# Optimization experiments

Hardware: AMD Instinct MI355X
Metric: run time of the kernel (lower is better)

The kernel has to match this reference:

```python
import jax, jax.numpy as jnp
import numpy as np

B, N, C, O = 512, 64, 256, 256  # batch graphs, agents(nodes), in_ch, out_ch


def _full_graph_edges(n):
    # PyG-style directed upper-triangular edges (j, i+j+1) + self loops,
    # then GCN symmetric normalization with in-degree computed at col.
    src, dst = np.triu_indices(n, k=1)           # src < dst, matches build_edge_index('full')
    loop = np.arange(n)
    row = np.concatenate([src, loop]).astype(np.int32)   # message source
    col = np.concatenate([dst, loop]).astype(np.int32)   # message target (aggregation)
    deg = np.bincount(col, minlength=n).astype(np.float32)
    dis = 1.0 / np.sqrt(deg)
    norm = (dis[row] * dis[col]).astype(np.float32)
    return jnp.asarray(row), jnp.asarray(col), jnp.asarray(norm)


def setup_inputs() -> dict:
    key = jax.random.key(0)
    k1, k2 = jax.random.split(key, 2)
    x = jax.random.normal(k1, (B, N, C), dtype=jnp.float32)
    W = jax.random.normal(k2, (C, O), dtype=jnp.float32) / np.sqrt(C)
    b = jnp.zeros((O,), dtype=jnp.float32)
    return {"x": x, "W": W, "b": b}


def reference(x, W, b):
    # GCNConv: out = D^-1/2 (A + I) D^-1/2 (X W) + b, then ReLU (module forward).
    n = x.shape[1]
    row, col, norm = _full_graph_edges(n)
    xw = jnp.einsum('bnc,co->bno', x, W)                      # [B, N, O]
    msg = xw[:, row, :] * norm[None, :, None]                 # gather along edges [B, E, O]
    agg = jax.vmap(lambda m: jax.ops.segment_sum(m, col, num_segments=n))(msg)  # scatter-add [B, N, O]
    return jax.nn.relu(agg + b)
```

## Files before the change

kernel.cpp:

```cpp
#include <hip/hip_runtime.h>


#define BATCH 512
#define NNODE 64
#define CIN   256
#define COUT  256

typedef __bf16 bf16x8 __attribute__((ext_vector_type(8)));
typedef float  f32x4  __attribute__((ext_vector_type(4)));

#define LGKM_BARRIER() asm volatile("s_waitcnt lgkmcnt(0)\n\ts_barrier" ::: "memory")

__global__ __launch_bounds__(512, 1) void gcn_fused(
    const float* __restrict__ X,
    const float* __restrict__ W,
    const float* __restrict__ bias,
    float* __restrict__ out)
{
    __shared__ uint4 Xs4[2][2048];
    const int tid  = threadIdx.x;
    const int lane = tid & 63;
    const int w    = tid >> 6;
    const int g    = lane >> 4;
    const int c    = lane & 15;
    const int colbase = w * 32;
    const int xg   = blockIdx.x * 2;

    const float* xb0 = X + (size_t)xg * (NNODE * CIN);
    const float* xb1 = xb0 + NNODE * CIN;

    f32x4 pf[8];
#pragma unroll
    for (int i = 0; i < 4; ++i) {
        int ch  = tid + i * 512;
        const f32x4* p = reinterpret_cast<const f32x4*>(
            xb0 + (ch >> 5) * CIN + ((ch & 31) << 3));
        pf[2 * i]     = p[0];
        pf[2 * i + 1] = p[1];
    }

    bf16x8 bfr[8][2];
    {
        const float* Wp = W + colbase + c;
#pragma unroll
        for (int kk = 0; kk < 8; ++kk)
#pragma unroll
            for (int nt = 0; nt < 2; ++nt) {
                bf16x8 t;
#pragma unroll
                for (int j = 0; j < 8; ++j)
                    t[j] = (__bf16)Wp[(size_t)(kk * 32 + g * 8 + j) * COUT + nt * 16];
                bfr[kk][nt] = t;
            }
    }
    float bias_c[2];
#pragma unroll
    for (int nt = 0; nt < 2; ++nt)
        bias_c[nt] = bias[colbase + nt * 16 + c];

#pragma unroll
    for (int i = 0; i < 4; ++i) {
        int ch  = tid + i * 512;
        int row = ch >> 5;
        int c8  = (ch & 31) << 3;
        f32x4 v0 = pf[2 * i], v1 = pf[2 * i + 1];
        bf16x8 h;
        h[0] = (__bf16)v0[0]; h[1] = (__bf16)v0[1];
        h[2] = (__bf16)v0[2]; h[3] = (__bf16)v0[3];
        h[4] = (__bf16)v1[0]; h[5] = (__bf16)v1[1];
        h[6] = (__bf16)v1[2]; h[7] = (__bf16)v1[3];
        int byte = (row << 9) + (c8 << 1);
        byte ^= (row & 7) << 4;
        *reinterpret_cast<uint4*>((unsigned char*)Xs4[0] + byte) =
            __builtin_bit_cast(uint4, h);
    }

    f32x4 pg[8];
#pragma unroll
    for (int i = 0; i < 4; ++i) {
        int ch  = tid + i * 512;
        const f32x4* p = reinterpret_cast<const f32x4*>(
            xb1 + (ch >> 5) * CIN + ((ch & 31) << 3));
        pg[2 * i]     = p[0];
        pg[2 * i + 1] = p[1];
    }

    float dd[4][4];
#pragma unroll
    for (int mt = 0; mt < 4; ++mt)
#pragma unroll
        for (int r = 0; r < 4; ++r)
            dd[mt][r] = rsqrtf((float)(mt * 16 + g * 4 + r + 1));

    const int swz = (c & 7) << 4;

    auto gemm = [&](const unsigned char* Xs, f32x4 (&acc)[4][2]) {
#pragma unroll
        for (int kk = 0; kk < 8; ++kk) {
            bf16x8 a[4];
#pragma unroll
            for (int mt = 0; mt < 4; ++mt) {
                int byte = ((mt * 16 + c) << 9) + (kk << 6) + (g << 4);
                byte ^= swz;
                a[mt] = *reinterpret_cast<const bf16x8*>(Xs + byte);
            }
#pragma unroll
            for (int mt = 0; mt < 4; ++mt)
#pragma unroll
                for (int nt = 0; nt < 2; ++nt)
                    acc[mt][nt] = __builtin_amdgcn_mfma_f32_16x16x32_bf16(
                        a[mt], bfr[kk][nt], acc[mt][nt], 0, 0, 0);
        }
    };

    auto epilogue = [&](f32x4 (&acc)[4][2], float* ob) {
        float t_[4][2];
#pragma unroll
        for (int mt = 0; mt < 4; ++mt)
#pragma unroll
            for (int nt = 0; nt < 2; ++nt) {
                f32x4 v = acc[mt][nt];
                v[0] *= dd[mt][0]; v[1] *= dd[mt][1];
                v[2] *= dd[mt][2]; v[3] *= dd[mt][3];
                v[1] += v[0]; v[2] += v[1]; v[3] += v[2];
                acc[mt][nt] = v;
                t_[mt][nt] = v[3];
            }
        float Ofs[4][2];
#pragma unroll
        for (int nt = 0; nt < 2; ++nt) {
            float run = 0.0f;
#pragma unroll
            for (int mt = 0; mt < 4; ++mt) {
                float v    = t_[mt][nt];
                float p    = __shfl_xor(v, 16, 64);
                float excl = (g & 1) ? p : 0.0f;
                float pair = v + p;
                float q    = __shfl_xor(pair, 32, 64);
                excl += (g & 2) ? q : 0.0f;
                Ofs[mt][nt] = run + excl;
                run += pair + q;
            }
        }
#pragma unroll
        for (int mt = 0; mt < 4; ++mt)
#pragma unroll
            for (int r = 0; r < 4; ++r) {
                const int row = mt * 16 + g * 4 + r;
                const float dr = dd[mt][r];
#pragma unroll
                for (int nt = 0; nt < 2; ++nt) {
                    float val = (acc[mt][nt][r] + Ofs[mt][nt]) * dr + bias_c[nt];
                    ob[row * COUT + nt * 16] = fmaxf(val, 0.0f);
                }
            }
    };

    LGKM_BARRIER();

    f32x4 acc0[4][2] = {};
    gemm((const unsigned char*)Xs4[0], acc0);

#pragma unroll
    for (int i = 0; i < 4; ++i) {
        int ch  = tid + i * 512;
        int row = ch >> 5;
        int c8  = (ch & 31) << 3;
        f32x4 v0 = pg[2 * i], v1 = pg[2 * i + 1];
        bf16x8 h;
        h[0] = (__bf16)v0[0]; h[1] = (__bf16)v0[1];
        h[2] = (__bf16)v0[2]; h[3] = (__bf16)v0[3];
        h[4] = (__bf16)v1[0]; h[5] = (__bf16)v1[1];
        h[6] = (__bf16)v1[2]; h[7] = (__bf16)v1[3];
        int byte = (row << 9) + (c8 << 1);
        byte ^= (row & 7) << 4;
        *reinterpret_cast<uint4*>((unsigned char*)Xs4[1] + byte) =
            __builtin_bit_cast(uint4, h);
    }

    epilogue(acc0, out + (size_t)xg * (NNODE * COUT) + colbase + c);

    LGKM_BARRIER();

    f32x4 acc1[4][2] = {};
    gemm((const unsigned char*)Xs4[1], acc1);
    epilogue(acc1, out + (size_t)(xg + 1) * (NNODE * COUT) + colbase + c);
}

extern "C" void kernel_launch(void* const* d_in, const int* in_sizes, int n_in,
                              void* d_out, int out_size, void* d_ws, size_t ws_size,
                              hipStream_t stream) {
    const float* x = (const float*)d_in[0];
    const float* W = (const float*)d_in[1];
    const float* bsp = (const float*)d_in[2];
    float* out = (float*)d_out;

    hipLaunchKernelGGL(gcn_fused, dim3(BATCH / 2), dim3(512), 0, stream,
                       x, W, bsp, out);
}
```

Before: 21.54 us.

## Pre-transpose W to bf16 in a prep kernel and defer second X prefetch

Adds a small prep kernel that converts W to bf16 and transposes it into the workspace, so each main-kernel thread can load its B fragments as contiguous 16-byte vectors instead of 128 strided scalar float loads. The prefetch of the second graph's X rows is also moved after the first barrier to reduce register pressure during the first conversion. The cost is an extra kernel launch that reads and writes W on every call, and the later prefetch may expose more of the X load latency.

Result: slower. 25.43 us (+18.1%).

```diff
diff --git a/kernel.cpp b/kernel.cpp
--- a/kernel.cpp
+++ b/kernel.cpp
@@ -9,11 +9,14 @@
 typedef __bf16 bf16x8 __attribute__((ext_vector_type(8)));
 typedef float  f32x4  __attribute__((ext_vector_type(4)));
 
-#define LGKM_BARRIER() asm volatile("s_waitcnt lgkmcnt(0)\n\ts_barrier" ::: "memory")
+__device__ __forceinline__ unsigned int f2bf_bits(float f) {
+    unsigned int u = __builtin_bit_cast(unsigned int, f);
+    return (u + 0x7fffu + ((u >> 16) & 1u)) >> 16;
+}
 
 __global__ __launch_bounds__(512, 1) void gcn_fused(
     const float* __restrict__ X,
-    const float* __restrict__ W,
+    const unsigned short* __restrict__ WT,
     const float* __restrict__ bias,
     float* __restrict__ out)
 {
@@ -41,17 +44,12 @@
 
     bf16x8 bfr[8][2];
     {
-        const float* Wp = W + colbase + c;
+        const unsigned short* WTb = WT + (size_t)(colbase + c) * CIN + g * 8;
 #pragma unroll
         for (int kk = 0; kk < 8; ++kk)
 #pragma unroll
-            for (int nt = 0; nt < 2; ++nt) {
-                bf16x8 t;
-#pragma unroll
-                for (int j = 0; j < 8; ++j)
-                    t[j] = (__bf16)Wp[(size_t)(kk * 32 + g * 8 + j) * COUT + nt * 16];
-                bfr[kk][nt] = t;
-            }
+            for (int nt = 0; nt < 2; ++nt)
+                bfr[kk][nt] = *reinterpret_cast<const bf16x8*>(WTb + nt * 16 * CIN + kk * 32);
     }
     float bias_c[2];
 #pragma unroll
@@ -75,16 +73,6 @@
             __builtin_bit_cast(uint4, h);
     }
 
-    f32x4 pg[8];
-#pragma unroll
-    for (int i = 0; i < 4; ++i) {
-        int ch  = tid + i * 512;
-        const f32x4* p = reinterpret_cast<const f32x4*>(
-            xb1 + (ch >> 5) * CIN + ((ch & 31) << 3));
-        pg[2 * i]     = p[0];
-        pg[2 * i + 1] = p[1];
-    }
-
     float dd[4][4];
 #pragma unroll
     for (int mt = 0; mt < 4; ++mt)
@@ -156,7 +144,17 @@
             }
     };
 
-    LGKM_BARRIER();
+    __syncthreads();
+
+    f32x4 pg[8];
+#pragma unroll
+    for (int i = 0; i < 4; ++i) {
+        int ch  = tid + i * 512;
+        const f32x4* p = reinterpret_cast<const f32x4*>(
+            xb1 + (ch >> 5) * CIN + ((ch & 31) << 3));
+        pg[2 * i]     = p[0];
+        pg[2 * i + 1] = p[1];
+    }
 
     f32x4 acc0[4][2] = {};
     gemm((const unsigned char*)Xs4[0], acc0);
@@ -180,11 +178,33 @@
 
     epilogue(acc0, out + (size_t)xg * (NNODE * COUT) + colbase + c);
 
-    LGKM_BARRIER();
+    __syncthreads();
 
     f32x4 acc1[4][2] = {};
     gemm((const unsigned char*)Xs4[1], acc1);
     epilogue(acc1, out + (size_t)(xg + 1) * (NNODE * COUT) + colbase + c);
+}
+
+__global__ void wprep(const float* __restrict__ W, unsigned short* __restrict__ Wt) {
+    __shared__ unsigned short tile[64][72];
+    const int tid = threadIdx.x;
+    const int tk  = blockIdx.x & 3;
+    const int tn  = blockIdx.x >> 2;
+#pragma unroll
+    for (int i = 0; i < 16; ++i) {
+        int idx = tid + i * 256;
+        int r  = idx >> 6;
+        int cc = idx & 63;
+        tile[cc][r] = (unsigned short)f2bf_bits(W[(tk * 64 + r) * 256 + tn * 64 + cc]);
+    }
+    __syncthreads();
+#pragma unroll
+    for (int i = 0; i < 16; ++i) {
+        int idx = tid + i * 256;
+        int rr = idx >> 6;
+        int cc = idx & 63;
+        Wt[(tn * 64 + rr) * 256 + tk * 64 + cc] = tile[rr][cc];
+    }
 }
 
 extern "C" void kernel_launch(void* const* d_in, const int* in_sizes, int n_in,
@@ -194,7 +214,9 @@
     const float* W = (const float*)d_in[1];
     const float* bsp = (const float*)d_in[2];
     float* out = (float*)d_out;
-
+    unsigned short* Wt = (unsigned short*)d_ws;
+
+    hipLaunchKernelGGL(wprep, dim3(16), dim3(256), 0, stream, W, Wt);
     hipLaunchKernelGGL(gcn_fused, dim3(BATCH / 2), dim3(512), 0, stream,
-                       x, W, bsp, out);
-}
+                       x, Wt, bsp, out);
+}
```
